# Kernel tuning notes

Hardware: AMD Instinct MI355X
Metric: run time of the kernel (lower is better)

## Reference

```python
import jax, jax.numpy as jnp
import numpy as np

MIN_NORM = 1e-15
PROJ_EPS = 4e-3  # hgcn PoincareBall eps for float32
C = 1.0          # curvature (c_in == c_out == 1.0)


def artanh(x):
    x = jnp.clip(x, -1.0 + 1e-7, 1.0 - 1e-7)
    return 0.5 * (jnp.log1p(x) - jnp.log1p(-x))


def _norm(x):
    return jnp.maximum(jnp.linalg.norm(x, axis=-1, keepdims=True), MIN_NORM)


def proj(x, c):
    norm = _norm(x)
    maxnorm = (1.0 - PROJ_EPS) / jnp.sqrt(c)
    return jnp.where(norm > maxnorm, x / norm * maxnorm, x)


def expmap0(u, c):
    sc = jnp.sqrt(c)
    un = _norm(u)
    return jnp.tanh(sc * un) * u / (sc * un)


def logmap0(p, c):
    sc = jnp.sqrt(c)
    pn = _norm(p)
    return artanh(sc * pn) * p / (sc * pn)


def mobius_add(x, y, c):
    x2 = jnp.sum(x * x, axis=-1, keepdims=True)
    y2 = jnp.sum(y * y, axis=-1, keepdims=True)
    xy = jnp.sum(x * y, axis=-1, keepdims=True)
    num = (1.0 + 2.0 * c * xy + c * y2) * x + (1.0 - c * x2) * y
    den = 1.0 + 2.0 * c * xy + c * c * x2 * y2
    return num / jnp.maximum(den, MIN_NORM)


def mobius_matvec(m, x, c):
    # m: [out, in], x: [N, in] on the Poincare ball
    sc = jnp.sqrt(c)
    xn = _norm(x)
    mx = x @ m.T                      # [N, out]
    mxn = _norm(mx)
    res = jnp.tanh(mxn / xn * artanh(sc * xn)) * mx / (mxn * sc)
    zero = jnp.all(mx == 0, axis=-1, keepdims=True)
    return jnp.where(zero, jnp.zeros_like(res), res)


def setup_inputs() -> dict:
    key = jax.random.key(0)
    ks = jax.random.split(key, 6)
    N, IN, OUT = 1546, 1546, 64
    # hyperbolic input features: expmap0 of a small tangent vector, then proj
    x_tan = jax.random.normal(ks[0], (N, IN), jnp.float32) * 0.01
    x = proj(expmap0(x_tan, C), C)
    adj = jax.random.uniform(ks[1], (N, N), jnp.float32)
    adj = adj / jnp.sum(adj, axis=1, keepdims=True)  # row-normalized adjacency
    xav = np.sqrt(2.0) * np.sqrt(2.0 / (IN + OUT))   # xavier_uniform std-ish scale
    W_drug = jax.random.normal(ks[2], (OUT, IN), jnp.float32) * xav
    W_micr = jax.random.normal(ks[3], (OUT, IN), jnp.float32) * xav
    bias_drug = jnp.zeros((OUT,), jnp.float32)
    bias_micr = jnp.zeros((OUT,), jnp.float32)
    wn_scale = np.sqrt(2.0) * np.sqrt(2.0 / (128 + 64))
    weightnode = jax.random.normal(ks[4], (128, 64), jnp.float32) * wn_scale
    biasnode = jnp.zeros((N, 1), jnp.float32)
    return {"x": x, "adj": adj, "W_drug": W_drug, "W_micr": W_micr,
            "bias_drug": bias_drug, "bias_micr": bias_micr,
            "weightnode": weightnode, "biasnode": biasnode}


def _hyp_linear(x, W, bias, c):
    mv = proj(mobius_matvec(W, x, c), c)
    hyp_bias = proj(expmap0(bias[None, :], c), c)  # proj_tan0 is identity on Poincare
    return proj(mobius_add(mv, hyp_bias, c), c)


def reference(x, adj, W_drug, W_micr, bias_drug, bias_micr, weightnode, biasnode):
    N_DRUG, N_MICR = 1373, 173
    # ---- HypLinear (x.shape[1] == 1546 branch) ----
    res_drug = _hyp_linear(x, W_drug, bias_drug, C)
    res_micr = _hyp_linear(x, W_micr, bias_micr, C)
    liner_h = jnp.concatenate([res_drug[:N_DRUG], res_micr[-N_MICR:]], axis=0)  # [1546, 64]
    # ---- HypAgg (use_att=False: spmm aggregation in tangent space at origin) ----
    x_tangent = logmap0(liner_h, C)          # [1546, 64]
    support_t = adj @ x_tangent              # [1546, 64]
    agg_h = proj(expmap0(support_t, C), C)
    # ---- HypAct (gated mix; the logmap0/expmap0 'result' is dead code, overwritten) ----
    zf = jnp.concatenate([agg_h, liner_h], axis=1)          # [1546, 128]
    delt1 = jax.nn.relu(zf @ weightnode + biasnode)         # [1546, 64]
    h = delt1 * agg_h + (1.0 - delt1) * liner_h
    return h, adj
```

## Files before the change

### kernel.cpp

```cpp
#include <hip/hip_runtime.h>
#include <math.h>

#define NROWS 1546
#define INDIM 1546
#define ODIM  64
#define NDRUG 1373
#define MINN  1e-15f
#define MAXNRM 0.996f

#define KS     4
#define KSTEPS 49
#define FRAGSZ (KSTEPS * 4 * 512)

typedef short  short8 __attribute__((ext_vector_type(8)));
typedef float  f32x4  __attribute__((ext_vector_type(4)));

__device__ __forceinline__ unsigned short f2bf(float f) {
    unsigned u = __float_as_uint(f);
    u += 0x7FFFu + ((u >> 16) & 1u);
    return (unsigned short)(u >> 16);
}

__device__ __forceinline__ float artanh_(float x) {
    x = fminf(fmaxf(x, -1.0f + 1e-7f), 1.0f - 1e-7f);
    return 0.5f * (log1pf(x) - log1pf(-x));
}

__device__ __forceinline__ float wsum(float v) {
#pragma unroll
    for (int off = 32; off > 0; off >>= 1) v += __shfl_xor(v, off, 64);
    return v;
}

__global__ void prep_kernel(const float* __restrict__ Wd, const float* __restrict__ Wm,
                            unsigned short* __restrict__ WfD, unsigned short* __restrict__ WfM,
                            const float* __restrict__ bd, const float* __restrict__ bm,
                            float* __restrict__ hbD, float* __restrict__ hbM,
                            float* __restrict__ hb2,
                            const float4* __restrict__ adj4, float4* __restrict__ adjout4,
                            int n4) {
    int tid = threadIdx.x;
    if (blockIdx.x < 64) {
        int total = 64 * 1568;
        for (int i = blockIdx.x * 256 + tid; i < total; i += 64 * 256) {
            int o = i / 1568, k = i - o * 1568;
            int kstep = k >> 5, rem = k & 31, lgrp = rem >> 3, j = rem & 7;
            int addr = (kstep * 4 + (o >> 4)) * 512 + (lgrp * 16 + (o & 15)) * 8 + j;
            float vd = (k < INDIM) ? Wd[o * INDIM + k] : 0.f;
            float vm = (k < INDIM) ? Wm[o * INDIM + k] : 0.f;
            WfD[addr] = f2bf(vd);
            WfM[addr] = f2bf(vm);
        }
        return;
    }
    if (blockIdx.x == 64) {
        if (tid < 128) {
            int wave = tid >> 6, lane = tid & 63;
            const float* b = wave ? bm : bd;
            float v = b[lane];
            float un2 = wsum(v * v);
            float un = fmaxf(sqrtf(un2), MINN);
            float e = tanhf(un) * v / un;
            float en2 = wsum(e * e);
            float en = fmaxf(sqrtf(en2), MINN);
            float scl = (en > MAXNRM) ? (MAXNRM / en) : 1.0f;
            float* hb = wave ? hbM : hbD;
            hb[lane] = e * scl;
            if (lane == 0) hb2[wave] = en2 * scl * scl;
        }
        return;
    }
    int nb = gridDim.x - 65;
    for (int i = (blockIdx.x - 65) * 256 + tid; i < n4; i += nb * 256)
        adjout4[i] = adj4[i];
}

__global__ __launch_bounds__(256) void gemm_liner_mfma(
    const float* __restrict__ X,
    const unsigned short* __restrict__ WfD, const unsigned short* __restrict__ WfM,
    float* __restrict__ part, float* __restrict__ pnorm) {
    int s = blockIdx.x;
    int strip = (s == 97) ? 85 : s;
    int rowbase = strip * 16;
    int kc = threadIdx.x >> 6, lane = threadIdx.x & 63;
    int lrow = lane & 15, lgrp = lane >> 4;
    const unsigned short* Bf = (s <= 85) ? WfD : WfM;
    int lo = (s == 97) ? NDRUG : 0;
    int hi = (s == 85) ? NDRUG : NROWS;
    const float* arow = X + (size_t)min(rowbase + lrow, NROWS - 1) * INDIM;

    f32x4 ac0 = {0,0,0,0}, ac1 = {0,0,0,0}, ac2 = {0,0,0,0}, ac3 = {0,0,0,0};
    float ss = 0.f;
    int ks0 = 12 * kc;
    int ks1 = 12 * kc + 12;
    for (int ks = ks0; ks < ks1; ++ks) {
        const float* xp = arow + ks * 32 + lgrp * 8;
        float2 p0 = *(const float2*)(xp);
        float2 p1 = *(const float2*)(xp + 2);
        float2 p2 = *(const float2*)(xp + 4);
        float2 p3 = *(const float2*)(xp + 6);
        float xv[8] = {p0.x, p0.y, p1.x, p1.y, p2.x, p2.y, p3.x, p3.y};
        short8 av;
#pragma unroll
        for (int j = 0; j < 8; ++j) { ss = fmaf(xv[j], xv[j], ss); av[j] = (short)f2bf(xv[j]); }
        const unsigned short* bp = Bf + (size_t)(ks * 4) * 512 + lane * 8;
        short8 b0 = *(const short8*)(bp);
        short8 b1 = *(const short8*)(bp + 512);
        short8 b2 = *(const short8*)(bp + 1024);
        short8 b3 = *(const short8*)(bp + 1536);
        ac0 = __builtin_amdgcn_mfma_f32_16x16x32_bf16(av, b0, ac0, 0, 0, 0);
        ac1 = __builtin_amdgcn_mfma_f32_16x16x32_bf16(av, b1, ac1, 0, 0, 0);
        ac2 = __builtin_amdgcn_mfma_f32_16x16x32_bf16(av, b2, ac2, 0, 0, 0);
        ac3 = __builtin_amdgcn_mfma_f32_16x16x32_bf16(av, b3, ac3, 0, 0, 0);
    }
    if (kc == 3) {
        short8 av;
#pragma unroll
        for (int j = 0; j < 8; ++j) {
            int k = 1536 + lgrp * 8 + j;
            float v = (k < INDIM) ? arow[k] : 0.f;
            ss = fmaf(v, v, ss);
            av[j] = (short)f2bf(v);
        }
        const unsigned short* bp = Bf + (size_t)(48 * 4) * 512 + lane * 8;
        short8 b0 = *(const short8*)(bp);
        short8 b1 = *(const short8*)(bp + 512);
        short8 b2 = *(const short8*)(bp + 1024);
        short8 b3 = *(const short8*)(bp + 1536);
        ac0 = __builtin_amdgcn_mfma_f32_16x16x32_bf16(av, b0, ac0, 0, 0, 0);
        ac1 = __builtin_amdgcn_mfma_f32_16x16x32_bf16(av, b1, ac1, 0, 0, 0);
        ac2 = __builtin_amdgcn_mfma_f32_16x16x32_bf16(av, b2, ac2, 0, 0, 0);
        ac3 = __builtin_amdgcn_mfma_f32_16x16x32_bf16(av, b3, ac3, 0, 0, 0);
    }
    ss += __shfl_xor(ss, 16, 64);
    ss += __shfl_xor(ss, 32, 64);
    if (s != 97 && lane < 16) {
        int r = rowbase + lrow;
        if (r < NROWS) pnorm[r * KS + kc] = ss;
    }
#pragma unroll
    for (int i = 0; i < 4; ++i) {
        int r = rowbase + lgrp * 4 + i;
        if (r >= lo && r < hi) {
            size_t base = (size_t)r * (KS * 64) + kc * 64 + lrow;
            part[base]      = ac0[i];
            part[base + 16] = ac1[i];
            part[base + 32] = ac2[i];
            part[base + 48] = ac3[i];
        }
    }
}

__global__ __launch_bounds__(512) void linerB(
    const float* __restrict__ part, const float* __restrict__ pnorm,
    const float* __restrict__ hbD, const float* __restrict__ hbM, const float* __restrict__ hb2v,
    float* __restrict__ liner, unsigned short* __restrict__ xtf) {
    int wave = threadIdx.x >> 6, lane = threadIdx.x & 63;
    int grow = blockIdx.x * 8 + wave;
    if (grow >= NROWS) {
        for (int row = grow; row < 1568; row += 6)
            xtf[((row >> 5) * 4 + (lane >> 4)) * 512 +
                (((row & 31) >> 3) * 16 + (lane & 15)) * 8 + (row & 7)] = 0;
        return;
    }
    float mx = 0.f, xn2 = 0.f;
#pragma unroll
    for (int kc = 0; kc < KS; ++kc) mx += part[(size_t)grow * (KS * 64) + kc * 64 + lane];
#pragma unroll
    for (int kc = 0; kc < KS; ++kc) xn2 += pnorm[grow * KS + kc];

    float mxn2 = wsum(mx * mx);
    float xn = fmaxf(sqrtf(xn2), MINN);
    float mxn = fmaxf(sqrtf(mxn2), MINN);
    float g = mxn / xn * artanh_(xn);
    float t = tanhf(g);
    float res = t * mx / mxn;
    float rn = fabsf(t);
    if (rn > MAXNRM) { res *= MAXNRM / rn; rn = MAXNRM; }
    const float* hb = (grow < NDRUG) ? hbD : hbM;
    float y = hb[lane];
    float y2 = hb2v[(grow < NDRUG) ? 0 : 1];
    float x2 = rn * rn;
    float xy = wsum(res * y);
    float num = (1.0f + 2.0f * xy + y2) * res + (1.0f - x2) * y;
    float den = 1.0f + 2.0f * xy + x2 * y2;
    float v = num / fmaxf(den, MINN);
    float v2 = wsum(v * v);
    float vn = fmaxf(sqrtf(v2), MINN);
    if (vn > MAXNRM) { v *= MAXNRM / vn; vn = MAXNRM; }
    float xt = artanh_(vn) / vn * v;
    liner[(size_t)grow * ODIM + lane] = v;
    xtf[((grow >> 5) * 4 + (lane >> 4)) * 512 +
        (((grow & 31) >> 3) * 16 + (lane & 15)) * 8 + (grow & 7)] = f2bf(xt);
}

__global__ __launch_bounds__(256) void gemm_agg_mfma(
    const float* __restrict__ ADJ, const unsigned short* __restrict__ xtf,
    float* __restrict__ part) {
    int rowbase = blockIdx.x * 16;
    int kc = threadIdx.x >> 6, lane = threadIdx.x & 63;
    int lrow = lane & 15, lgrp = lane >> 4;
    const float* arow = ADJ + (size_t)min(rowbase + lrow, NROWS - 1) * INDIM;

    f32x4 ac0 = {0,0,0,0}, ac1 = {0,0,0,0}, ac2 = {0,0,0,0}, ac3 = {0,0,0,0};
    int ks0 = 12 * kc;
    int ks1 = 12 * kc + 12;
    for (int ks = ks0; ks < ks1; ++ks) {
        const float* xp = arow + ks * 32 + lgrp * 8;
        float2 p0 = *(const float2*)(xp);
        float2 p1 = *(const float2*)(xp + 2);
        float2 p2 = *(const float2*)(xp + 4);
        float2 p3 = *(const float2*)(xp + 6);
        float xv[8] = {p0.x, p0.y, p1.x, p1.y, p2.x, p2.y, p3.x, p3.y};
        short8 av;
#pragma unroll
        for (int j = 0; j < 8; ++j) av[j] = (short)f2bf(xv[j]);
        const unsigned short* bp = xtf + (size_t)(ks * 4) * 512 + lane * 8;
        short8 b0 = *(const short8*)(bp);
        short8 b1 = *(const short8*)(bp + 512);
        short8 b2 = *(const short8*)(bp + 1024);
        short8 b3 = *(const short8*)(bp + 1536);
        ac0 = __builtin_amdgcn_mfma_f32_16x16x32_bf16(av, b0, ac0, 0, 0, 0);
        ac1 = __builtin_amdgcn_mfma_f32_16x16x32_bf16(av, b1, ac1, 0, 0, 0);
        ac2 = __builtin_amdgcn_mfma_f32_16x16x32_bf16(av, b2, ac2, 0, 0, 0);
        ac3 = __builtin_amdgcn_mfma_f32_16x16x32_bf16(av, b3, ac3, 0, 0, 0);
    }
    if (kc == 3) {
        short8 av;
#pragma unroll
        for (int j = 0; j < 8; ++j) {
            int k = 1536 + lgrp * 8 + j;
            av[j] = (short)f2bf((k < INDIM) ? arow[k] : 0.f);
        }
        const unsigned short* bp = xtf + (size_t)(48 * 4) * 512 + lane * 8;
        short8 b0 = *(const short8*)(bp);
        short8 b1 = *(const short8*)(bp + 512);
        short8 b2 = *(const short8*)(bp + 1024);
        short8 b3 = *(const short8*)(bp + 1536);
        ac0 = __builtin_amdgcn_mfma_f32_16x16x32_bf16(av, b0, ac0, 0, 0, 0);
        ac1 = __builtin_amdgcn_mfma_f32_16x16x32_bf16(av, b1, ac1, 0, 0, 0);
        ac2 = __builtin_amdgcn_mfma_f32_16x16x32_bf16(av, b2, ac2, 0, 0, 0);
        ac3 = __builtin_amdgcn_mfma_f32_16x16x32_bf16(av, b3, ac3, 0, 0, 0);
    }
#pragma unroll
    for (int i = 0; i < 4; ++i) {
        int r = rowbase + lgrp * 4 + i;
        if (r < NROWS) {
            size_t base = (size_t)r * (KS * 64) + kc * 64 + lrow;
            part[base]      = ac0[i];
            part[base + 16] = ac1[i];
            part[base + 32] = ac2[i];
            part[base + 48] = ac3[i];
        }
    }
}

__global__ __launch_bounds__(512) void aggB(
    const float* __restrict__ part, const float* __restrict__ liner,
    const float* __restrict__ WN , const float* __restrict__ biasnode,
    float* __restrict__ out_h) {
    __shared__ float zl[8][128];
    int wave = threadIdx.x >> 6, lane = threadIdx.x & 63;
    int grow = blockIdx.x * 8 + wave;
    if (grow >= NROWS) return;
    float s = 0.f;
#pragma unroll
    for (int kc = 0; kc < KS; ++kc) s += part[(size_t)grow * (KS * 64) + kc * 64 + lane];
    float sn2 = wsum(s * s);
    float sn = fmaxf(sqrtf(sn2), MINN);
    float th = tanhf(sn);
    float agg = th * s / sn;
    if (th > MAXNRM) agg *= MAXNRM / th;
    float lin = liner[(size_t)grow * ODIM + lane];
    zl[wave][lane] = agg;
    zl[wave][64 + lane] = lin;
    float d = biasnode[grow];
    const float* w = WN + lane;
#pragma unroll 8
    for (int f = 0; f < 128; ++f) d = fmaf(zl[wave][f], w[f * 64], d);
    d = fmaxf(d, 0.0f);
    out_h[(size_t)grow * ODIM + lane] = d * agg + (1.0f - d) * lin;
}

extern "C" void kernel_launch(void* const* d_in, const int* in_sizes, int n_in,
                              void* d_out, int out_size, void* d_ws, size_t ws_size,
                              hipStream_t stream) {
    const float* x   = (const float*)d_in[0];
    const float* adj = (const float*)d_in[1];
    const float* Wd  = (const float*)d_in[2];
    const float* Wm  = (const float*)d_in[3];
    const float* bd  = (const float*)d_in[4];
    const float* bm  = (const float*)d_in[5];
    const float* wn  = (const float*)d_in[6];
    const float* bn  = (const float*)d_in[7];
    float* out = (float*)d_out;

    const int WELEMS = ODIM * INDIM;
    unsigned short* WfD = (unsigned short*)d_ws;
    unsigned short* WfM = WfD + FRAGSZ;
    unsigned short* xtf = WfM + FRAGSZ;
    float* hbD   = (float*)(xtf + FRAGSZ);
    float* hbM   = hbD + 64;
    float* hb2   = hbM + 64;
    float* liner = hbD + 192;
    float* pnorm = liner + WELEMS;
    float* part  = pnorm + 6184;

    int n4 = (NROWS * NROWS) / 4;
    prep_kernel<<<512, 256, 0, stream>>>(Wd, Wm, WfD, WfM, bd, bm, hbD, hbM, hb2,
                                         (const float4*)adj, (float4*)(out + WELEMS), n4);
    gemm_liner_mfma<<<98, 256, 0, stream>>>(x, WfD, WfM, part, pnorm);
    linerB<<<194, 512, 0, stream>>>(part, pnorm, hbD, hbM, hb2, liner, xtf);
    gemm_agg_mfma<<<97, 256, 0, stream>>>(adj, xtf, part);
    aggB<<<194, 512, 0, stream>>>(part, liner, wn, bn, out);
}
```

Before: 35.85 us.

## Fuse split-K GEMMs with their epilogues via shared-memory reduction

Merges each split-K MFMA GEMM with its row-wise epilogue kernel. Partial sums now reduce through shared memory inside one block instead of a global partial buffer, and the split-K factor rises from 4 to 8 waves per block (512 threads), with K steps interleaved across waves. This removes two kernel launches and the global round trips for partial sums and norms. In exchange each block uses more LDS, and only 2 rows per wave are left for the epilogue after a block-wide barrier.

New measurement: 35.59 us. No clear change (-0.7%).

```diff
diff --git a/kernel.cpp b/kernel.cpp
--- a/kernel.cpp
+++ b/kernel.cpp
@@ -8,9 +8,9 @@
 #define MINN  1e-15f
 #define MAXNRM 0.996f
 
-#define KS     4
 #define KSTEPS 49
 #define FRAGSZ (KSTEPS * 4 * 512)
+#define REDS   65
 
 typedef short  short8 __attribute__((ext_vector_type(8)));
 typedef float  f32x4  __attribute__((ext_vector_type(4)));
@@ -19,6 +19,10 @@
     unsigned u = __float_as_uint(f);
     u += 0x7FFFu + ((u >> 16) & 1u);
     return (unsigned short)(u >> 16);
+}
+
+__device__ __forceinline__ int fragaddr(int k, int col) {
+    return ((k >> 5) * 4 + (col >> 4)) * 512 + (((k & 31) >> 3) * 16 + (col & 15)) * 8 + (k & 7);
 }
 
 __device__ __forceinline__ float artanh_(float x) {
@@ -44,8 +48,7 @@
         int total = 64 * 1568;
         for (int i = blockIdx.x * 256 + tid; i < total; i += 64 * 256) {
             int o = i / 1568, k = i - o * 1568;
-            int kstep = k >> 5, rem = k & 31, lgrp = rem >> 3, j = rem & 7;
-            int addr = (kstep * 4 + (o >> 4)) * 512 + (lgrp * 16 + (o & 15)) * 8 + j;
+            int addr = fragaddr(k, o);
             float vd = (k < INDIM) ? Wd[o * INDIM + k] : 0.f;
             float vm = (k < INDIM) ? Wm[o * INDIM + k] : 0.f;
             WfD[addr] = f2bf(vd);
@@ -75,15 +78,18 @@
         adjout4[i] = adj4[i];
 }
 
-__global__ __launch_bounds__(256) void gemm_liner_mfma(
+__global__ __launch_bounds__(512) void liner_fused(
     const float* __restrict__ X,
     const unsigned short* __restrict__ WfD, const unsigned short* __restrict__ WfM,
-    float* __restrict__ part, float* __restrict__ pnorm) {
+    const float* __restrict__ hbD, const float* __restrict__ hbM, const float* __restrict__ hb2v,
+    float* __restrict__ liner, unsigned short* __restrict__ xtf) {
+    __shared__ float red[8][16][REDS];
+    __shared__ float ssl[8][16];
+    int tid = threadIdx.x, kc = tid >> 6, lane = tid & 63;
+    int lrow = lane & 15, lgrp = lane >> 4;
     int s = blockIdx.x;
     int strip = (s == 97) ? 85 : s;
     int rowbase = strip * 16;
-    int kc = threadIdx.x >> 6, lane = threadIdx.x & 63;
-    int lrow = lane & 15, lgrp = lane >> 4;
     const unsigned short* Bf = (s <= 85) ? WfD : WfM;
     int lo = (s == 97) ? NDRUG : 0;
     int hi = (s == 85) ? NDRUG : NROWS;
@@ -91,9 +97,7 @@
 
     f32x4 ac0 = {0,0,0,0}, ac1 = {0,0,0,0}, ac2 = {0,0,0,0}, ac3 = {0,0,0,0};
     float ss = 0.f;
-    int ks0 = 12 * kc;
-    int ks1 = 12 * kc + 12;
-    for (int ks = ks0; ks < ks1; ++ks) {
+    for (int ks = kc; ks < 48; ks += 8) {
         const float* xp = arow + ks * 32 + lgrp * 8;
         float2 p0 = *(const float2*)(xp);
         float2 p1 = *(const float2*)(xp + 2);
@@ -113,7 +117,7 @@
         ac2 = __builtin_amdgcn_mfma_f32_16x16x32_bf16(av, b2, ac2, 0, 0, 0);
         ac3 = __builtin_amdgcn_mfma_f32_16x16x32_bf16(av, b3, ac3, 0, 0, 0);
     }
-    if (kc == 3) {
+    if (kc == 0) {
         short8 av;
 #pragma unroll
         for (int j = 0; j < 8; ++j) {
@@ -134,78 +138,68 @@
     }
     ss += __shfl_xor(ss, 16, 64);
     ss += __shfl_xor(ss, 32, 64);
-    if (s != 97 && lane < 16) {
-        int r = rowbase + lrow;
-        if (r < NROWS) pnorm[r * KS + kc] = ss;
-    }
+    if (lane < 16) ssl[kc][lrow] = ss;
 #pragma unroll
     for (int i = 0; i < 4; ++i) {
-        int r = rowbase + lgrp * 4 + i;
-        if (r >= lo && r < hi) {
-            size_t base = (size_t)r * (KS * 64) + kc * 64 + lrow;
-            part[base]      = ac0[i];
-            part[base + 16] = ac1[i];
-            part[base + 32] = ac2[i];
-            part[base + 48] = ac3[i];
-        }
-    }
-}
-
-__global__ __launch_bounds__(512) void linerB(
-    const float* __restrict__ part, const float* __restrict__ pnorm,
-    const float* __restrict__ hbD, const float* __restrict__ hbM, const float* __restrict__ hb2v,
-    float* __restrict__ liner, unsigned short* __restrict__ xtf) {
-    int wave = threadIdx.x >> 6, lane = threadIdx.x & 63;
-    int grow = blockIdx.x * 8 + wave;
-    if (grow >= NROWS) {
-        for (int row = grow; row < 1568; row += 6)
-            xtf[((row >> 5) * 4 + (lane >> 4)) * 512 +
-                (((row & 31) >> 3) * 16 + (lane & 15)) * 8 + (row & 7)] = 0;
-        return;
-    }
-    float mx = 0.f, xn2 = 0.f;
-#pragma unroll
-    for (int kc = 0; kc < KS; ++kc) mx += part[(size_t)grow * (KS * 64) + kc * 64 + lane];
-#pragma unroll
-    for (int kc = 0; kc < KS; ++kc) xn2 += pnorm[grow * KS + kc];
-
-    float mxn2 = wsum(mx * mx);
-    float xn = fmaxf(sqrtf(xn2), MINN);
-    float mxn = fmaxf(sqrtf(mxn2), MINN);
-    float g = mxn / xn * artanh_(xn);
-    float t = tanhf(g);
-    float res = t * mx / mxn;
-    float rn = fabsf(t);
-    if (rn > MAXNRM) { res *= MAXNRM / rn; rn = MAXNRM; }
-    const float* hb = (grow < NDRUG) ? hbD : hbM;
-    float y = hb[lane];
-    float y2 = hb2v[(grow < NDRUG) ? 0 : 1];
-    float x2 = rn * rn;
-    float xy = wsum(res * y);
-    float num = (1.0f + 2.0f * xy + y2) * res + (1.0f - x2) * y;
-    float den = 1.0f + 2.0f * xy + x2 * y2;
-    float v = num / fmaxf(den, MINN);
-    float v2 = wsum(v * v);
-    float vn = fmaxf(sqrtf(v2), MINN);
-    if (vn > MAXNRM) { v *= MAXNRM / vn; vn = MAXNRM; }
-    float xt = artanh_(vn) / vn * v;
-    liner[(size_t)grow * ODIM + lane] = v;
-    xtf[((grow >> 5) * 4 + (lane >> 4)) * 512 +
-        (((grow & 31) >> 3) * 16 + (lane & 15)) * 8 + (grow & 7)] = f2bf(xt);
-}
-
-__global__ __launch_bounds__(256) void gemm_agg_mfma(
+        int r = lgrp * 4 + i;
+        red[kc][r][lrow]      = ac0[i];
+        red[kc][r][16 + lrow] = ac1[i];
+        red[kc][r][32 + lrow] = ac2[i];
+        red[kc][r][48 + lrow] = ac3[i];
+    }
+    __syncthreads();
+
+#pragma unroll
+    for (int j = 0; j < 2; ++j) {
+        int r = 2 * kc + j;
+        int grow = rowbase + r;
+        if (grow >= lo && grow < hi) {
+            float mx = 0.f, xn2 = 0.f;
+#pragma unroll
+            for (int w = 0; w < 8; ++w) { mx += red[w][r][lane]; xn2 += ssl[w][r]; }
+            float mxn2 = wsum(mx * mx);
+            float xn = fmaxf(sqrtf(xn2), MINN);
+            float mxn = fmaxf(sqrtf(mxn2), MINN);
+            float g = mxn / xn * artanh_(xn);
+            float t = tanhf(g);
+            float res = t * mx / mxn;
+            float rn = fabsf(t);
+            if (rn > MAXNRM) { res *= MAXNRM / rn; rn = MAXNRM; }
+            const float* hb = (grow < NDRUG) ? hbD : hbM;
+            float y = hb[lane];
+            float y2 = hb2v[(grow < NDRUG) ? 0 : 1];
+            float x2 = rn * rn;
+            float xy = wsum(res * y);
+            float num = (1.0f + 2.0f * xy + y2) * res + (1.0f - x2) * y;
+            float den = 1.0f + 2.0f * xy + x2 * y2;
+            float v = num / fmaxf(den, MINN);
+            float v2 = wsum(v * v);
+            float vn = fmaxf(sqrtf(v2), MINN);
+            if (vn > MAXNRM) { v *= MAXNRM / vn; vn = MAXNRM; }
+            float xt = artanh_(vn) / vn * v;
+            liner[(size_t)grow * ODIM + lane] = v;
+            xtf[fragaddr(grow, lane)] = f2bf(xt);
+        }
+    }
+    if (s == 96) {
+        for (int row = NROWS + kc; row < 1568; row += 8)
+            xtf[fragaddr(row, lane)] = 0;
+    }
+}
+
+__global__ __launch_bounds__(512) void agg_fused(
     const float* __restrict__ ADJ, const unsigned short* __restrict__ xtf,
-    float* __restrict__ part) {
+    const float* __restrict__ liner, const float* __restrict__ WN ,
+    const float* __restrict__ biasnode, float* __restrict__ out_h) {
+    __shared__ float red[8][16][REDS];
+    __shared__ float zl[16][128];
+    int tid = threadIdx.x, kc = tid >> 6, lane = tid & 63;
+    int lrow = lane & 15, lgrp = lane >> 4;
     int rowbase = blockIdx.x * 16;
-    int kc = threadIdx.x >> 6, lane = threadIdx.x & 63;
-    int lrow = lane & 15, lgrp = lane >> 4;
     const float* arow = ADJ + (size_t)min(rowbase + lrow, NROWS - 1) * INDIM;
 
     f32x4 ac0 = {0,0,0,0}, ac1 = {0,0,0,0}, ac2 = {0,0,0,0}, ac3 = {0,0,0,0};
-    int ks0 = 12 * kc;
-    int ks1 = 12 * kc + 12;
-    for (int ks = ks0; ks < ks1; ++ks) {
+    for (int ks = kc; ks < 48; ks += 8) {
         const float* xp = arow + ks * 32 + lgrp * 8;
         float2 p0 = *(const float2*)(xp);
         float2 p1 = *(const float2*)(xp + 2);
@@ -225,7 +219,7 @@
         ac2 = __builtin_amdgcn_mfma_f32_16x16x32_bf16(av, b2, ac2, 0, 0, 0);
         ac3 = __builtin_amdgcn_mfma_f32_16x16x32_bf16(av, b3, ac3, 0, 0, 0);
     }
-    if (kc == 3) {
+    if (kc == 0) {
         short8 av;
 #pragma unroll
         for (int j = 0; j < 8; ++j) {
@@ -244,42 +238,38 @@
     }
 #pragma unroll
     for (int i = 0; i < 4; ++i) {
-        int r = rowbase + lgrp * 4 + i;
-        if (r < NROWS) {
-            size_t base = (size_t)r * (KS * 64) + kc * 64 + lrow;
-            part[base]      = ac0[i];
-            part[base + 16] = ac1[i];
-            part[base + 32] = ac2[i];
-            part[base + 48] = ac3[i];
-        }
-    }
-}
-
-__global__ __launch_bounds__(512) void aggB(
-    const float* __restrict__ part, const float* __restrict__ liner,
-    const float* __restrict__ WN , const float* __restrict__ biasnode,
-    float* __restrict__ out_h) {
-    __shared__ float zl[8][128];
-    int wave = threadIdx.x >> 6, lane = threadIdx.x & 63;
-    int grow = blockIdx.x * 8 + wave;
-    if (grow >= NROWS) return;
-    float s = 0.f;
-#pragma unroll
-    for (int kc = 0; kc < KS; ++kc) s += part[(size_t)grow * (KS * 64) + kc * 64 + lane];
-    float sn2 = wsum(s * s);
-    float sn = fmaxf(sqrtf(sn2), MINN);
-    float th = tanhf(sn);
-    float agg = th * s / sn;
-    if (th > MAXNRM) agg *= MAXNRM / th;
-    float lin = liner[(size_t)grow * ODIM + lane];
-    zl[wave][lane] = agg;
-    zl[wave][64 + lane] = lin;
-    float d = biasnode[grow];
-    const float* w = WN + lane;
+        int r = lgrp * 4 + i;
+        red[kc][r][lrow]      = ac0[i];
+        red[kc][r][16 + lrow] = ac1[i];
+        red[kc][r][32 + lrow] = ac2[i];
+        red[kc][r][48 + lrow] = ac3[i];
+    }
+    __syncthreads();
+
+#pragma unroll
+    for (int j = 0; j < 2; ++j) {
+        int r = 2 * kc + j;
+        int grow = rowbase + r;
+        if (grow < NROWS) {
+            float sv = 0.f;
+#pragma unroll
+            for (int w = 0; w < 8; ++w) sv += red[w][r][lane];
+            float sn2 = wsum(sv * sv);
+            float sn = fmaxf(sqrtf(sn2), MINN);
+            float th = tanhf(sn);
+            float agg = th * sv / sn;
+            if (th > MAXNRM) agg *= MAXNRM / th;
+            float lin = liner[(size_t)grow * ODIM + lane];
+            zl[r][lane] = agg;
+            zl[r][64 + lane] = lin;
+            float d = biasnode[grow];
+            const float* w = WN + lane;
 #pragma unroll 8
-    for (int f = 0; f < 128; ++f) d = fmaf(zl[wave][f], w[f * 64], d);
-    d = fmaxf(d, 0.0f);
-    out_h[(size_t)grow * ODIM + lane] = d * agg + (1.0f - d) * lin;
+            for (int f = 0; f < 128; ++f) d = fmaf(zl[r][f], w[f * 64], d);
+            d = fmaxf(d, 0.0f);
+            out_h[(size_t)grow * ODIM + lane] = d * agg + (1.0f - d) * lin;
+        }
+    }
 }
 
 extern "C" void kernel_launch(void* const* d_in, const int* in_sizes, int n_in,
@@ -303,14 +293,10 @@
     float* hbM   = hbD + 64;
     float* hb2   = hbM + 64;
     float* liner = hbD + 192;
-    float* pnorm = liner + WELEMS;
-    float* part  = pnorm + 6184;
 
     int n4 = (NROWS * NROWS) / 4;
     prep_kernel<<<512, 256, 0, stream>>>(Wd, Wm, WfD, WfM, bd, bm, hbD, hbM, hb2,
                                          (const float4*)adj, (float4*)(out + WELEMS), n4);
-    gemm_liner_mfma<<<98, 256, 0, stream>>>(x, WfD, WfM, part, pnorm);
-    linerB<<<194, 512, 0, stream>>>(part, pnorm, hbD, hbM, hb2, liner, xtf);
-    gemm_agg_mfma<<<97, 256, 0, stream>>>(adj, xtf, part);
-    aggB<<<194, 512, 0, stream>>>(part, liner, wn, bn, out);
-}
+    liner_fused<<<98, 512, 0, stream>>>(x, WfD, WfM, hbD, hbM, hb2, liner, xtf);
+    agg_fused<<<97, 512, 0, stream>>>(adj, xtf, liner, wn, bn, out);
+}
```

## Split GEMM K dimension across two blocks with in-block LDS reduction

Applied to the files above, without the earlier changes.

Both MFMA GEMM kernels now launch a 2D grid: each strip is split into two halves of the K range, so each block's 4 waves cover interleaved k-steps of 8-way split-K. Partial accumulators are reduced across waves through shared memory before being written, which halves the per-row partial buffer and the reads in linerB/aggB. This doubles the number of blocks on a GPU with many CUs to improve occupancy, at the cost of an LDS round-trip and a __syncthreads.

After: 33.06 us. -7.8%, faster.

```diff
diff --git a/kernel.cpp b/kernel.cpp
--- a/kernel.cpp
+++ b/kernel.cpp
@@ -8,9 +8,9 @@
 #define MINN  1e-15f
 #define MAXNRM 0.996f
 
-#define KS     4
 #define KSTEPS 49
 #define FRAGSZ (KSTEPS * 4 * 512)
+#define REDS   65
 
 typedef short  short8 __attribute__((ext_vector_type(8)));
 typedef float  f32x4  __attribute__((ext_vector_type(4)));
@@ -19,6 +19,10 @@
     unsigned u = __float_as_uint(f);
     u += 0x7FFFu + ((u >> 16) & 1u);
     return (unsigned short)(u >> 16);
+}
+
+__device__ __forceinline__ int fragaddr(int k, int col) {
+    return ((k >> 5) * 4 + (col >> 4)) * 512 + (((k & 31) >> 3) * 16 + (col & 15)) * 8 + (k & 7);
 }
 
 __device__ __forceinline__ float artanh_(float x) {
@@ -44,8 +48,7 @@
         int total = 64 * 1568;
         for (int i = blockIdx.x * 256 + tid; i < total; i += 64 * 256) {
             int o = i / 1568, k = i - o * 1568;
-            int kstep = k >> 5, rem = k & 31, lgrp = rem >> 3, j = rem & 7;
-            int addr = (kstep * 4 + (o >> 4)) * 512 + (lgrp * 16 + (o & 15)) * 8 + j;
+            int addr = fragaddr(k, o);
             float vd = (k < INDIM) ? Wd[o * INDIM + k] : 0.f;
             float vm = (k < INDIM) ? Wm[o * INDIM + k] : 0.f;
             WfD[addr] = f2bf(vd);
@@ -79,11 +82,15 @@
     const float* __restrict__ X,
     const unsigned short* __restrict__ WfD, const unsigned short* __restrict__ WfM,
     float* __restrict__ part, float* __restrict__ pnorm) {
+    __shared__ float red[4][16][REDS];
+    __shared__ float ssl[4][16];
+    int tid = threadIdx.x, wave = tid >> 6, lane = tid & 63;
+    int lrow = lane & 15, lgrp = lane >> 4;
     int s = blockIdx.x;
+    int h = blockIdx.y;
+    int kc = h * 4 + wave;
     int strip = (s == 97) ? 85 : s;
     int rowbase = strip * 16;
-    int kc = threadIdx.x >> 6, lane = threadIdx.x & 63;
-    int lrow = lane & 15, lgrp = lane >> 4;
     const unsigned short* Bf = (s <= 85) ? WfD : WfM;
     int lo = (s == 97) ? NDRUG : 0;
     int hi = (s == 85) ? NDRUG : NROWS;
@@ -91,9 +98,7 @@
 
     f32x4 ac0 = {0,0,0,0}, ac1 = {0,0,0,0}, ac2 = {0,0,0,0}, ac3 = {0,0,0,0};
     float ss = 0.f;
-    int ks0 = 12 * kc;
-    int ks1 = 12 * kc + 12;
-    for (int ks = ks0; ks < ks1; ++ks) {
+    for (int ks = kc; ks < 48; ks += 8) {
         const float* xp = arow + ks * 32 + lgrp * 8;
         float2 p0 = *(const float2*)(xp);
         float2 p1 = *(const float2*)(xp + 2);
@@ -113,7 +118,7 @@
         ac2 = __builtin_amdgcn_mfma_f32_16x16x32_bf16(av, b2, ac2, 0, 0, 0);
         ac3 = __builtin_amdgcn_mfma_f32_16x16x32_bf16(av, b3, ac3, 0, 0, 0);
     }
-    if (kc == 3) {
+    if (kc == 0) {
         short8 av;
 #pragma unroll
         for (int j = 0; j < 8; ++j) {
@@ -134,19 +139,27 @@
     }
     ss += __shfl_xor(ss, 16, 64);
     ss += __shfl_xor(ss, 32, 64);
-    if (s != 97 && lane < 16) {
-        int r = rowbase + lrow;
-        if (r < NROWS) pnorm[r * KS + kc] = ss;
-    }
+    if (lane < 16) ssl[wave][lrow] = ss;
 #pragma unroll
     for (int i = 0; i < 4; ++i) {
-        int r = rowbase + lgrp * 4 + i;
-        if (r >= lo && r < hi) {
-            size_t base = (size_t)r * (KS * 64) + kc * 64 + lrow;
-            part[base]      = ac0[i];
-            part[base + 16] = ac1[i];
-            part[base + 32] = ac2[i];
-            part[base + 48] = ac3[i];
+        int r = lgrp * 4 + i;
+        red[wave][r][lrow]      = ac0[i];
+        red[wave][r][16 + lrow] = ac1[i];
+        red[wave][r][32 + lrow] = ac2[i];
+        red[wave][r][48 + lrow] = ac3[i];
+    }
+    __syncthreads();
+
+#pragma unroll
+    for (int j = 0; j < 4; ++j) {
+        int r = wave * 4 + j;
+        int grow = rowbase + r;
+        if (grow >= lo && grow < hi) {
+            float p = red[0][r][lane] + red[1][r][lane] + red[2][r][lane] + red[3][r][lane];
+            part[(size_t)(grow * 2 + h) * 64 + lane] = p;
+        }
+        if (s != 97 && grow < NROWS && lane == 0) {
+            pnorm[grow * 2 + h] = ssl[0][r] + ssl[1][r] + ssl[2][r] + ssl[3][r];
         }
     }
 }
@@ -159,15 +172,11 @@
     int grow = blockIdx.x * 8 + wave;
     if (grow >= NROWS) {
         for (int row = grow; row < 1568; row += 6)
-            xtf[((row >> 5) * 4 + (lane >> 4)) * 512 +
-                (((row & 31) >> 3) * 16 + (lane & 15)) * 8 + (row & 7)] = 0;
+            xtf[fragaddr(row, lane)] = 0;
         return;
     }
-    float mx = 0.f, xn2 = 0.f;
-#pragma unroll
-    for (int kc = 0; kc < KS; ++kc) mx += part[(size_t)grow * (KS * 64) + kc * 64 + lane];
-#pragma unroll
-    for (int kc = 0; kc < KS; ++kc) xn2 += pnorm[grow * KS + kc];
+    float mx = part[(size_t)(grow * 2) * 64 + lane] + part[(size_t)(grow * 2 + 1) * 64 + lane];
+    float xn2 = pnorm[grow * 2] + pnorm[grow * 2 + 1];
 
     float mxn2 = wsum(mx * mx);
     float xn = fmaxf(sqrtf(xn2), MINN);
@@ -190,22 +199,22 @@
     if (vn > MAXNRM) { v *= MAXNRM / vn; vn = MAXNRM; }
     float xt = artanh_(vn) / vn * v;
     liner[(size_t)grow * ODIM + lane] = v;
-    xtf[((grow >> 5) * 4 + (lane >> 4)) * 512 +
-        (((grow & 31) >> 3) * 16 + (lane & 15)) * 8 + (grow & 7)] = f2bf(xt);
+    xtf[fragaddr(grow, lane)] = f2bf(xt);
 }
 
 __global__ __launch_bounds__(256) void gemm_agg_mfma(
     const float* __restrict__ ADJ, const unsigned short* __restrict__ xtf,
     float* __restrict__ part) {
+    __shared__ float red[4][16][REDS];
+    int tid = threadIdx.x, wave = tid >> 6, lane = tid & 63;
+    int lrow = lane & 15, lgrp = lane >> 4;
     int rowbase = blockIdx.x * 16;
-    int kc = threadIdx.x >> 6, lane = threadIdx.x & 63;
-    int lrow = lane & 15, lgrp = lane >> 4;
+    int h = blockIdx.y;
+    int kc = h * 4 + wave;
     const float* arow = ADJ + (size_t)min(rowbase + lrow, NROWS - 1) * INDIM;
 
     f32x4 ac0 = {0,0,0,0}, ac1 = {0,0,0,0}, ac2 = {0,0,0,0}, ac3 = {0,0,0,0};
-    int ks0 = 12 * kc;
-    int ks1 = 12 * kc + 12;
-    for (int ks = ks0; ks < ks1; ++ks) {
+    for (int ks = kc; ks < 48; ks += 8) {
         const float* xp = arow + ks * 32 + lgrp * 8;
         float2 p0 = *(const float2*)(xp);
         float2 p1 = *(const float2*)(xp + 2);
@@ -225,7 +234,7 @@
         ac2 = __builtin_amdgcn_mfma_f32_16x16x32_bf16(av, b2, ac2, 0, 0, 0);
         ac3 = __builtin_amdgcn_mfma_f32_16x16x32_bf16(av, b3, ac3, 0, 0, 0);
     }
-    if (kc == 3) {
+    if (kc == 0) {
         short8 av;
 #pragma unroll
         for (int j = 0; j < 8; ++j) {
@@ -244,13 +253,21 @@
     }
 #pragma unroll
     for (int i = 0; i < 4; ++i) {
-        int r = rowbase + lgrp * 4 + i;
-        if (r < NROWS) {
-            size_t base = (size_t)r * (KS * 64) + kc * 64 + lrow;
-            part[base]      = ac0[i];
-            part[base + 16] = ac1[i];
-            part[base + 32] = ac2[i];
-            part[base + 48] = ac3[i];
+        int r = lgrp * 4 + i;
+        red[wave][r][lrow]      = ac0[i];
+        red[wave][r][16 + lrow] = ac1[i];
+        red[wave][r][32 + lrow] = ac2[i];
+        red[wave][r][48 + lrow] = ac3[i];
+    }
+    __syncthreads();
+
+#pragma unroll
+    for (int j = 0; j < 4; ++j) {
+        int r = wave * 4 + j;
+        int grow = rowbase + r;
+        if (grow < NROWS) {
+            float p = red[0][r][lane] + red[1][r][lane] + red[2][r][lane] + red[3][r][lane];
+            part[(size_t)(grow * 2 + h) * 64 + lane] = p;
         }
     }
 }
@@ -263,9 +280,7 @@
     int wave = threadIdx.x >> 6, lane = threadIdx.x & 63;
     int grow = blockIdx.x * 8 + wave;
     if (grow >= NROWS) return;
-    float s = 0.f;
-#pragma unroll
-    for (int kc = 0; kc < KS; ++kc) s += part[(size_t)grow * (KS * 64) + kc * 64 + lane];
+    float s = part[(size_t)(grow * 2) * 64 + lane] + part[(size_t)(grow * 2 + 1) * 64 + lane];
     float sn2 = wsum(s * s);
     float sn = fmaxf(sqrtf(sn2), MINN);
     float th = tanhf(sn);
@@ -304,13 +319,13 @@
     float* hb2   = hbM + 64;
     float* liner = hbD + 192;
     float* pnorm = liner + WELEMS;
-    float* part  = pnorm + 6184;
+    float* part  = pnorm + 3092;
 
     int n4 = (NROWS * NROWS) / 4;
     prep_kernel<<<512, 256, 0, stream>>>(Wd, Wm, WfD, WfM, bd, bm, hbD, hbM, hb2,
                                          (const float4*)adj, (float4*)(out + WELEMS), n4);
-    gemm_liner_mfma<<<98, 256, 0, stream>>>(x, WfD, WfM, part, pnorm);
+    gemm_liner_mfma<<<dim3(98, 2), 256, 0, stream>>>(x, WfD, WfM, part, pnorm);
     linerB<<<194, 512, 0, stream>>>(part, pnorm, hbD, hbM, hb2, liner, xtf);
-    gemm_agg_mfma<<<97, 256, 0, stream>>>(adj, xtf, part);
+    gemm_agg_mfma<<<dim3(97, 2), 256, 0, stream>>>(adj, xtf, part);
     aggB<<<194, 512, 0, stream>>>(part, liner, wn, bn, out);
 }
```
